# Kernel optimization log

Measured on AMD Instinct MI355X. Metric: run time of the kernel, lower is better.

## Reference

```python
import jax, jax.numpy as jnp
import numpy as np

P = 7            # cfg.POOLING_SIZE (= group_size)
N_CLASSES = 21   # PASCAL VOC incl. background
SPATIAL_SCALE = 1.0 / 16.0


def _round_half_up(x):
    # matches C round() for non-negative roi coords (jnp.round is banker's)
    return jnp.floor(x + 0.5)


def psroi_pool(feat, rois, out_dim):
    """Position-sensitive RoI average pooling via integral images.
    feat: [B, out_dim*P*P, H, W]; rois: [N, 5] (batch_idx, x1, y1, x2, y2).
    Returns [N, out_dim, P, P]."""
    B, C, H, W = feat.shape
    # summed-area table, zero-padded: S[b,c,h,w] = sum feat[b,c,:h,:w]
    S = jnp.cumsum(jnp.cumsum(feat, axis=2), axis=3)
    S = jnp.pad(S, ((0, 0), (0, 0), (1, 0), (1, 0)))

    b = rois[:, 0].astype(jnp.int32)
    x1 = _round_half_up(rois[:, 1]) * SPATIAL_SCALE
    y1 = _round_half_up(rois[:, 2]) * SPATIAL_SCALE
    x2 = _round_half_up(rois[:, 3] + 1.0) * SPATIAL_SCALE
    y2 = _round_half_up(rois[:, 4] + 1.0) * SPATIAL_SCALE
    roi_w = jnp.maximum(x2 - x1, 0.1)
    roi_h = jnp.maximum(y2 - y1, 0.1)
    bin_w = roi_w / P
    bin_h = roi_h / P

    g = jnp.arange(P, dtype=feat.dtype)
    hs = jnp.clip(jnp.floor(g[None] * bin_h[:, None] + y1[:, None]), 0, H).astype(jnp.int32)        # [N,P]
    he = jnp.clip(jnp.ceil((g[None] + 1.0) * bin_h[:, None] + y1[:, None]), 0, H).astype(jnp.int32)
    ws = jnp.clip(jnp.floor(g[None] * bin_w[:, None] + x1[:, None]), 0, W).astype(jnp.int32)
    we = jnp.clip(jnp.ceil((g[None] + 1.0) * bin_w[:, None] + x1[:, None]), 0, W).astype(jnp.int32)

    # channel for (ctop, gh, gw) is (ctop*P + gh)*P + gw == arange(C) reshaped
    c = jnp.arange(C, dtype=jnp.int32).reshape(1, out_dim, P, P)
    bi = b[:, None, None, None]
    h0 = hs[:, None, :, None]; h1 = he[:, None, :, None]
    w0 = ws[:, None, None, :]; w1 = we[:, None, None, :]
    # box-sum from integral image -> [N, out_dim, P, P]
    ssum = S[bi, c, h1, w1] - S[bi, c, h0, w1] - S[bi, c, h1, w0] + S[bi, c, h0, w0]

    dh = jnp.maximum(he - hs, 0)[:, None, :, None]
    dw = jnp.maximum(we - ws, 0)[:, None, None, :]
    area = (dh * dw).astype(feat.dtype)
    return jnp.where(area > 0, ssum / jnp.maximum(area, 1.0), 0.0)


def setup_inputs() -> dict:
    key = jax.random.key(0)
    k1, k2, k3, k4, k5 = jax.random.split(key, 5)
    B, Cin, H, W = 4, 2048, 64, 64
    base_feat = jax.random.normal(k1, (B, Cin, H, W), jnp.float32)
    w_conv1 = 0.01 * jax.random.normal(k2, (1024, Cin), jnp.float32)
    w_cls = 0.01 * jax.random.normal(k3, (N_CLASSES * P * P, 1024), jnp.float32)
    w_bbox = 0.001 * jax.random.normal(k4, (4 * N_CLASSES * P * P, 1024), jnp.float32)
    # 300 ROIs per image in image coords (image size = 16*H = 1024)
    n_per = 300
    ka, kb = jax.random.split(k5)
    xy1 = jax.random.uniform(ka, (B * n_per, 2), jnp.float32, 0.0, 900.0)
    wh = jax.random.uniform(kb, (B * n_per, 2), jnp.float32, 16.0, 160.0)
    xy2 = jnp.minimum(xy1 + wh, 1023.0)
    bidx = jnp.repeat(jnp.arange(B, dtype=jnp.float32), n_per)[:, None]
    rois = jnp.concatenate([bidx, xy1[:, 0:1], xy1[:, 1:2], xy2[:, 0:1], xy2[:, 1:2]], axis=1)
    return {"base_feat": base_feat, "rois": rois, "w_conv1": w_conv1, "w_cls": w_cls, "w_bbox": w_bbox}


def reference(base_feat, rois, w_conv1, w_cls, w_bbox):
    B = base_feat.shape[0]
    n_per = rois.shape[0] // B
    # 1x1 conv (no bias) + relu
    x = jax.nn.relu(jnp.einsum('oi,bihw->bohw', w_conv1, base_feat))
    # cls branch: 1x1 conv -> PSRoIPool -> PxP avgpool -> softmax
    cls_feat = jnp.einsum('oi,bihw->bohw', w_cls, x)
    pooled_cls = psroi_pool(cls_feat, rois, N_CLASSES)        # [N, 21, P, P]
    cls_score = pooled_cls.mean(axis=(2, 3))                   # [N, 21]
    cls_prob = jax.nn.softmax(cls_score, axis=1)
    # bbox branch: 1x1 conv -> PSRoIPool -> PxP avgpool
    bbox_feat = jnp.einsum('oi,bihw->bohw', w_bbox, x)
    pooled_loc = psroi_pool(bbox_feat, rois, 4 * N_CLASSES)    # [N, 84, P, P]
    bbox_pred = pooled_loc.mean(axis=(2, 3))                    # [N, 84]
    return cls_prob.reshape(B, n_per, -1), bbox_pred.reshape(B, n_per, -1)
```

## Files before the change

kernel.cpp:

```cpp
#include <hip/hip_runtime.h>
#include <cstdint>


typedef __attribute__((ext_vector_type(8))) short short8;
typedef __attribute__((ext_vector_type(4))) short short4v;
typedef __attribute__((ext_vector_type(4))) float f32x4;

#define OFF_FEATT 0ull
#define OFF_W1    67108864ull
#define OFF_X     71303168ull
#define OFF_WC    104857600ull
#define OFF_DESC  117702656ull
#define OFF_P     0ull

__device__ __forceinline__ unsigned short f2bf(float f) {
  unsigned u = __float_as_uint(f);
  u += 0x7fffu + ((u >> 16) & 1u);
  return (unsigned short)(u >> 16);
}
__device__ __forceinline__ float bf2f(unsigned short h) {
  return __uint_as_float(((unsigned)h) << 16);
}

__device__ __forceinline__ int swz6(int k6, int key) {
  return ((((k6 >> 3) & 7) ^ key) << 3) | (k6 & 7);
}

__device__ __forceinline__ void gload16(const void* g, void* l) {
  __builtin_amdgcn_global_load_lds((const __attribute__((address_space(1))) void*)g,
                                   (__attribute__((address_space(3))) void*)l, 16, 0, 0);
}

__global__ __launch_bounds__(256) void k_prep(const float* __restrict__ w_conv1,
                                              const float* __restrict__ wcls,
                                              const float* __restrict__ wbbox,
                                              const float* __restrict__ rois,
                                              const float* __restrict__ base_feat,
                                              unsigned short* __restrict__ w1b,
                                              unsigned short* __restrict__ Wc,
                                              int* __restrict__ desc,
                                              unsigned short* __restrict__ featT) {
  __shared__ float tile2[2][64][65];
  int bid = blockIdx.x;
  if (bid < 2048) {
    int t = bid * 256 + threadIdx.x;
    long e = (long)t * 4;
    int o = (int)(e >> 11), k = (int)(e & 2047);
    float4 q = *(const float4*)(w_conv1 + e);
    short4v s = {(short)f2bf(q.x), (short)f2bf(q.y), (short)f2bf(q.z), (short)f2bf(q.w)};
    int kp = (k & ~63) | swz6(k & 63, o & 7);
    *(short4v*)(w1b + (size_t)o * 2048 + kp) = s;
  } else if (bid < 8320) {
    int t = (bid - 2048) * 256 + threadIdx.x;
    size_t e = (size_t)t * 4;
    int c = (int)(e / 50176);
    int rem = (int)(e - (size_t)c * 50176);
    int ij = rem >> 10, k = rem & 1023;
    float4 q = make_float4(0.f, 0.f, 0.f, 0.f);
    if (c < 21)       q = *(const float4*)(wcls + (size_t)(c * 49 + ij) * 1024 + k);
    else if (c < 105) q = *(const float4*)(wbbox + (size_t)((c - 21) * 49 + ij) * 1024 + k);
    short4v s = {(short)f2bf(q.x), (short)f2bf(q.y), (short)f2bf(q.z), (short)f2bf(q.w)};
    int kp = (k & ~63) | swz6(k & 63, c & 7);
    *(short4v*)(Wc + ((size_t)(c * 49 + ij) * 1024 + kp)) = s;
  } else if (bid < 8565) {
    int t = (bid - 8320) * 256 + threadIdx.x;
    if (t >= 1280 * 49) return;
    int roi = t / 49, ij = t - roi * 49;
    int* d = desc + (size_t)t * 8;
    if (roi >= 1200) { d[0] = 0; d[1] = 0; d[2] = 0; d[3] = 0; d[4] = 0; ((float*)d)[5] = 0.f; return; }
    const float* r = rois + (size_t)roi * 5;
    int b = (int)r[0];
    float x1 = __fmul_rn(floorf(__fadd_rn(r[1], 0.5f)), 0.0625f);
    float y1 = __fmul_rn(floorf(__fadd_rn(r[2], 0.5f)), 0.0625f);
    float x2 = __fmul_rn(floorf(__fadd_rn(__fadd_rn(r[3], 1.0f), 0.5f)), 0.0625f);
    float y2 = __fmul_rn(floorf(__fadd_rn(__fadd_rn(r[4], 1.0f), 0.5f)), 0.0625f);
    float bw = __fdiv_rn(fmaxf(__fsub_rn(x2, x1), 0.1f), 7.0f);
    float bh = __fdiv_rn(fmaxf(__fsub_rn(y2, y1), 0.1f), 7.0f);
    int i = ij / 7, j = ij - (ij / 7) * 7;
    float fi = (float)i, fj = (float)j;
    int hs = (int)fminf(fmaxf(floorf(__fadd_rn(__fmul_rn(fi, bh), y1)), 0.f), 64.f);
    int he = (int)fminf(fmaxf(ceilf(__fadd_rn(__fmul_rn(__fadd_rn(fi, 1.f), bh), y1)), 0.f), 64.f);
    int wsx = (int)fminf(fmaxf(floorf(__fadd_rn(__fmul_rn(fj, bw), x1)), 0.f), 64.f);
    int we = (int)fminf(fmaxf(ceilf(__fadd_rn(__fmul_rn(__fadd_rn(fj, 1.f), bw), x1)), 0.f), 64.f);
    int dh = max(he - hs, 0), dw = max(we - wsx, 0);
    float inv = (dh * dw > 0) ? 1.0f / (float)(dh * dw) : 0.f;
    d[0] = b; d[1] = hs; d[2] = he; d[3] = wsx; d[4] = we;
    ((float*)d)[5] = inv;
  } else {
    int t = bid - 8565;
    int s0 = (t & 31) * 128;
    int c0 = ((t >> 5) & 31) * 64;
    int b = t >> 10;
    int tx4 = (threadIdx.x & 15) * 4;
    int cl0 = threadIdx.x >> 4;
    const float* sp = base_feat + ((size_t)b * 2048 + c0) * 4096 + s0;
    float4 q[8];
#pragma unroll
    for (int tt = 0; tt < 2; tt++)
#pragma unroll
      for (int i = 0; i < 4; i++) {
        int cl = i * 16 + cl0;
        q[tt * 4 + i] = *(const float4*)(sp + (size_t)cl * 4096 + tt * 64 + tx4);
      }
#pragma unroll
    for (int tt = 0; tt < 2; tt++)
#pragma unroll
      for (int i = 0; i < 4; i++)
        *(float4*)&tile2[tt][i * 16 + cl0][tx4] = q[tt * 4 + i];
    __syncthreads();
    int c8 = (threadIdx.x & 7) * 8;
    int sy = threadIdx.x >> 3;
#pragma unroll
    for (int tt = 0; tt < 2; tt++) {
      unsigned short* dp = featT + ((size_t)b * 4096 + s0 + tt * 64) * 2048 + c0;
#pragma unroll
      for (int i = 0; i < 2; i++) {
        int sl = i * 32 + sy;
        int key = sl & 7;
        short8 v = {(short)f2bf(tile2[tt][c8 + 0][sl]), (short)f2bf(tile2[tt][c8 + 1][sl]),
                    (short)f2bf(tile2[tt][c8 + 2][sl]), (short)f2bf(tile2[tt][c8 + 3][sl]),
                    (short)f2bf(tile2[tt][c8 + 4][sl]), (short)f2bf(tile2[tt][c8 + 5][sl]),
                    (short)f2bf(tile2[tt][c8 + 6][sl]), (short)f2bf(tile2[tt][c8 + 7][sl])};
        *(short8*)(dp + (size_t)sl * 2048 + ((((c8 >> 3) ^ key) << 3))) = v;
      }
    }
  }
}

__global__ __launch_bounds__(512, 2) void k_gemm_conv1(const short* __restrict__ A,
                                                       const short* __restrict__ Bw,
                                                       unsigned short* __restrict__ X) {
  __shared__ short lds[9 * 8192];
  int mt = blockIdx.x, nt = blockIdx.y;
  int tid = threadIdx.x, lane = tid & 63, wave = tid >> 6;
  int wm = wave >> 2, wn = wave & 3;

  const short* Ab = A + (size_t)mt * 256 * 2048;
  const short* Bb = Bw + (size_t)nt * 256 * 2048;

  f32x4 acc[8][4];
#pragma unroll
  for (int i = 0; i < 8; i++)
#pragma unroll
    for (int j = 0; j < 4; j++) acc[i][j] = (f32x4){0.f, 0.f, 0.f, 0.f};

  int sr = tid >> 3;
  int sc = (tid & 7) * 8;
  auto stage_half = [&](int h) {
    if (h >= 128) return;
    int kind = h & 3, tl = h >> 2, slot = h % 9;
    const short* src = ((kind & 2) ? Bb : Ab)
                     + (size_t)((kind & 1) * 128 + sr) * 2048 + tl * 64 + sc;
    char* dst = (char*)lds + slot * 16384 + tid * 16;
    gload16(src, dst);
    gload16(src + (size_t)64 * 2048, dst + 8192);
  };

#pragma unroll
  for (int h = 0; h < 5; h++) stage_half(h);

  int la15 = lane & 15;
  int key = lane & 7;
  int ko0 = (((lane >> 4)) ^ key) << 3;
  int ko1 = ((4 | (lane >> 4)) ^ key) << 3;
  int bro = (wn & 1) * 64;

  for (int t = 0; t < 32; ++t) {
    if (t < 31) asm volatile("s_waitcnt vmcnt(2)" ::: "memory");
    else        asm volatile("s_waitcnt vmcnt(0)" ::: "memory");
    __builtin_amdgcn_s_barrier();
    __builtin_amdgcn_sched_barrier(0);
    const short* Asl = lds + (size_t)((4 * t + wm) % 9) * 8192;
    const short* Bsl = lds + (size_t)((4 * t + 2 + (wn >> 1)) % 9) * 8192;
    short8 af[4], bf[4];

    stage_half(4 * t + 5);
#pragma unroll
    for (int j = 0; j < 4; j++)
      bf[j] = *(const short8*)(Bsl + (bro + j * 16 + la15) * 64 + ko0);
#pragma unroll
    for (int i = 0; i < 4; i++)
      af[i] = *(const short8*)(Asl + (i * 16 + la15) * 64 + ko0);
    __builtin_amdgcn_s_setprio(1);
#pragma unroll
    for (int i = 0; i < 4; i++)
#pragma unroll
      for (int j = 0; j < 4; j++)
        acc[i][j] = __builtin_amdgcn_mfma_f32_16x16x32_bf16(af[i], bf[j], acc[i][j], 0, 0, 0);
    __builtin_amdgcn_s_setprio(0);

    stage_half(4 * t + 6);
#pragma unroll
    for (int i = 0; i < 4; i++)
      af[i] = *(const short8*)(Asl + (64 + i * 16 + la15) * 64 + ko0);
    __builtin_amdgcn_s_setprio(1);
#pragma unroll
    for (int i = 0; i < 4; i++)
#pragma unroll
      for (int j = 0; j < 4; j++)
        acc[4 + i][j] = __builtin_amdgcn_mfma_f32_16x16x32_bf16(af[i], bf[j], acc[4 + i][j], 0, 0, 0);
    __builtin_amdgcn_s_setprio(0);

    stage_half(4 * t + 7);
#pragma unroll
    for (int j = 0; j < 4; j++)
      bf[j] = *(const short8*)(Bsl + (bro + j * 16 + la15) * 64 + ko1);
#pragma unroll
    for (int i = 0; i < 4; i++)
      af[i] = *(const short8*)(Asl + (i * 16 + la15) * 64 + ko1);
    __builtin_amdgcn_s_setprio(1);
#pragma unroll
    for (int i = 0; i < 4; i++)
#pragma unroll
      for (int j = 0; j < 4; j++)
        acc[i][j] = __builtin_amdgcn_mfma_f32_16x16x32_bf16(af[i], bf[j], acc[i][j], 0, 0, 0);
    __builtin_amdgcn_s_setprio(0);

    stage_half(4 * t + 8);
#pragma unroll
    for (int i = 0; i < 4; i++)
      af[i] = *(const short8*)(Asl + (64 + i * 16 + la15) * 64 + ko1);
    __builtin_amdgcn_s_setprio(1);
#pragma unroll
    for (int i = 0; i < 4; i++)
#pragma unroll
      for (int j = 0; j < 4; j++)
        acc[4 + i][j] = __builtin_amdgcn_mfma_f32_16x16x32_bf16(af[i], bf[j], acc[4 + i][j], 0, 0, 0);
    __builtin_amdgcn_s_setprio(0);
  }

  unsigned short* Xo = X + ((size_t)(mt * 256 + wm * 128)) * 1024 + nt * 256 + wn * 64;
#pragma unroll
  for (int ii = 0; ii < 8; ii++)
#pragma unroll
    for (int j = 0; j < 4; j++) {
      int row = ii * 16 + (lane >> 4) * 4;
      int col = j * 16 + la15;
#pragma unroll
      for (int r = 0; r < 4; r++)
        Xo[(size_t)(row + r) * 1024 + col] = f2bf(fmaxf(acc[ii][j][r], 0.f));
    }
}

__global__ __launch_bounds__(512) void k_fusedpool(const unsigned short* __restrict__ Xb,
                                                   const int* __restrict__ desc,
                                                   const unsigned short* __restrict__ Wc,
                                                   unsigned short* __restrict__ P,
                                                   int nroi) {
  int mt = blockIdx.x;
  int ij = blockIdx.y;
  int kh = blockIdx.z;
  __shared__ short As[64 * 64];
  __shared__ short Bs[128 * 64];
  __shared__ int dsc[64][4];
  int tid = threadIdx.x, lane = tid & 63, wave = tid >> 6;

  if (tid < 64) {
    const int* d = desc + ((size_t)(mt * 64 + tid) * 49 + ij) * 8;
    int b = d[0], hs = d[1], he = d[2], wsx = d[3], we = d[4];
    dsc[tid][0] = (b * 64 + hs) * 64 + wsx;
    dsc[tid][1] = max(he - hs, 0);
    dsc[tid][2] = max(we - wsx, 0);
    dsc[tid][3] = d[5];
  }
  __syncthreads();

  f32x4 acc[4];
#pragma unroll
  for (int i = 0; i < 4; i++) acc[i] = (f32x4){0.f, 0.f, 0.f, 0.f};

  const unsigned short* Bb = Wc + (size_t)ij * 1024;
  int lr = lane >> 3, lc = (lane & 7) * 8;
  int key = lane & 7;
  int la15 = lane & 15;
  int r64 = tid >> 3;
  int k8 = tid & 7;
  int cs = dsc[r64][0], dh = dsc[r64][1], dw = dsc[r64][2];
  float inv = __int_as_float(dsc[r64][3]);
  int aswz = r64 * 64 + ((k8 ^ (r64 & 7)) << 3);

  int kbeg = kh * 512, kend = kbeg + 512;
  for (int k0 = kbeg; k0 < kend; k0 += 64) {
    const unsigned short* xp = Xb + (size_t)cs * 1024 + k0 + k8 * 8;
    short8 v[9];
#pragma unroll
    for (int hh = 0; hh < 3; hh++)
#pragma unroll
      for (int ww = 0; ww < 3; ww++) {
        int ho = (hh < dh) ? hh : 0;
        int wo = (ww < dw) ? ww : 0;
        v[hh * 3 + ww] = *(const short8*)(xp + (size_t)(ho * 64 + wo) * 1024);
      }
    {
      int row = wave * 8 + lr;
      gload16(Bb + (size_t)row * (49 * 1024) + k0 + lc, (char*)Bs + wave * 1024);
      gload16(Bb + (size_t)(row + 64) * (49 * 1024) + k0 + lc, (char*)Bs + 8192 + wave * 1024);
    }
    float a0 = 0.f, a1 = 0.f, a2 = 0.f, a3 = 0.f;
    float a4 = 0.f, a5 = 0.f, a6 = 0.f, a7 = 0.f;
#pragma unroll
    for (int hh = 0; hh < 3; hh++)
#pragma unroll
      for (int ww = 0; ww < 3; ww++) {
        float m = ((hh < dh) && (ww < dw)) ? inv : 0.f;
        short8 vv = v[hh * 3 + ww];
        a0 = fmaf(m, bf2f((unsigned short)vv[0]), a0);
        a1 = fmaf(m, bf2f((unsigned short)vv[1]), a1);
        a2 = fmaf(m, bf2f((unsigned short)vv[2]), a2);
        a3 = fmaf(m, bf2f((unsigned short)vv[3]), a3);
        a4 = fmaf(m, bf2f((unsigned short)vv[4]), a4);
        a5 = fmaf(m, bf2f((unsigned short)vv[5]), a5);
        a6 = fmaf(m, bf2f((unsigned short)vv[6]), a6);
        a7 = fmaf(m, bf2f((unsigned short)vv[7]), a7);
      }
    short8 o = {(short)f2bf(a0), (short)f2bf(a1), (short)f2bf(a2), (short)f2bf(a3),
                (short)f2bf(a4), (short)f2bf(a5), (short)f2bf(a6), (short)f2bf(a7)};
    *(short8*)(As + aswz) = o;
    __syncthreads();
#pragma unroll
    for (int kt = 0; kt < 2; kt++) {
      int ko = (((kt << 2) | (lane >> 4)) ^ key) << 3;
      short8 bfr = *(const short8*)(Bs + (wave * 16 + la15) * 64 + ko);
      short8 af[4];
#pragma unroll
      for (int i = 0; i < 4; i++)
        af[i] = *(const short8*)(As + (i * 16 + la15) * 64 + ko);
#pragma unroll
      for (int i = 0; i < 4; i++)
        acc[i] = __builtin_amdgcn_mfma_f32_16x16x32_bf16(af[i], bfr, acc[i], 0, 0, 0);
    }
    __syncthreads();
  }
  unsigned short* Pb = P + (size_t)(kh * 49 + ij) * nroi * 112;
  int cc = wave * 16 + la15;
  if (cc < 112) {
#pragma unroll
    for (int i = 0; i < 4; i++) {
      int rbase = mt * 64 + i * 16 + (lane >> 4) * 4;
#pragma unroll
      for (int r = 0; r < 4; r++)
        Pb[(size_t)(rbase + r) * 112 + cc] = f2bf(acc[i][r]);
    }
  }
}

__global__ __launch_bounds__(128) void k_redfinal(const unsigned short* __restrict__ P,
                                                  float* __restrict__ out, int nroi) {
  int roi = blockIdx.x;
  int c = threadIdx.x;
  __shared__ float sc[112];
  __shared__ float es[32];
  if (c < 112) {
    const unsigned short* p = P + (size_t)roi * 112 + c;
    float s = 0.f;
#pragma unroll 7
    for (int ij = 0; ij < 98; ij++) s += bf2f(p[(size_t)ij * nroi * 112]);
    sc[c] = s * (1.f / 49.f);
  }
  __syncthreads();
  if (c < 21) {
    float mx = -1e30f;
#pragma unroll
    for (int k = 0; k < 21; k++) mx = fmaxf(mx, sc[k]);
    es[c] = expf(sc[c] - mx);
  }
  __syncthreads();
  if (c < 21) {
    float sum = 0.f;
#pragma unroll
    for (int k = 0; k < 21; k++) sum += es[k];
    float rs = 1.f / sum;
    out[(size_t)roi * 21 + c] = es[c] * rs;
  }
  if (c >= 21 && c < 105) {
    out[25200 + (size_t)roi * 84 + (c - 21)] = sc[c];
  }
}

extern "C" void kernel_launch(void* const* d_in, const int* in_sizes, int n_in,
                              void* d_out, int out_size, void* d_ws, size_t ws_size,
                              hipStream_t stream) {
  const float* base_feat = (const float*)d_in[0];
  const float* rois      = (const float*)d_in[1];
  const float* w_conv1   = (const float*)d_in[2];
  const float* w_cls     = (const float*)d_in[3];
  const float* w_bbox    = (const float*)d_in[4];
  float* out = (float*)d_out;
  char* ws = (char*)d_ws;

  unsigned short* featT = (unsigned short*)(ws + OFF_FEATT);
  unsigned short* w1b   = (unsigned short*)(ws + OFF_W1);
  unsigned short* X     = (unsigned short*)(ws + OFF_X);
  unsigned short* Wc    = (unsigned short*)(ws + OFF_WC);
  int*            desc  = (int*)(ws + OFF_DESC);
  unsigned short* P     = (unsigned short*)(ws + OFF_P);

  k_prep<<<12661, 256, 0, stream>>>(w_conv1, w_cls, w_bbox, rois, base_feat,
                                    w1b, Wc, desc, featT);
  k_gemm_conv1<<<dim3(64, 4), 512, 0, stream>>>((const short*)featT, (const short*)w1b, X);
  k_fusedpool<<<dim3(20, 49, 2), 512, 0, stream>>>(X, desc, Wc, P, 1280);
  k_redfinal<<<1200, 128, 0, stream>>>(P, out, 1280);
}
```

Baseline: 356.1 us.

## Double-buffer fused pool-GEMM loads with register prefetch and LDS ping-pong

Restructures the k-loop of the fused PSRoI pooling + GEMM kernel into a software pipeline. The next k-step's nine X gathers are prefetched into registers and the next B tile is written into an alternate LDS buffer while the current step computes. Fixed per-thread masks and offsets are hoisted out of the loop, and s_setprio is raised around the MFMAs. The intent is to hide global load latency behind compute. It doubles LDS use and register pressure, and relies on hand-written vmcnt waits whose correctness depends on exact load counts.

```diff
diff --git a/kernel.cpp b/kernel.cpp
--- a/kernel.cpp
+++ b/kernel.cpp
@@ -250,8 +250,8 @@
   int mt = blockIdx.x;
   int ij = blockIdx.y;
   int kh = blockIdx.z;
-  __shared__ short As[64 * 64];
-  __shared__ short Bs[128 * 64];
+  __shared__ short As[2 * 4096];
+  __shared__ short Bs[2 * 8192];
   __shared__ int dsc[64][4];
   int tid = threadIdx.x, lane = tid & 63, wave = tid >> 6;
 
@@ -278,58 +278,87 @@
   int cs = dsc[r64][0], dh = dsc[r64][1], dw = dsc[r64][2];
   float inv = __int_as_float(dsc[r64][3]);
   int aswz = r64 * 64 + ((k8 ^ (r64 & 7)) << 3);
-
-  int kbeg = kh * 512, kend = kbeg + 512;
-  for (int k0 = kbeg; k0 < kend; k0 += 64) {
-    const unsigned short* xp = Xb + (size_t)cs * 1024 + k0 + k8 * 8;
-    short8 v[9];
-#pragma unroll
-    for (int hh = 0; hh < 3; hh++)
-#pragma unroll
-      for (int ww = 0; ww < 3; ww++) {
-        int ho = (hh < dh) ? hh : 0;
-        int wo = (ww < dw) ? ww : 0;
-        v[hh * 3 + ww] = *(const short8*)(xp + (size_t)(ho * 64 + wo) * 1024);
-      }
-    {
-      int row = wave * 8 + lr;
-      gload16(Bb + (size_t)row * (49 * 1024) + k0 + lc, (char*)Bs + wave * 1024);
-      gload16(Bb + (size_t)(row + 64) * (49 * 1024) + k0 + lc, (char*)Bs + 8192 + wave * 1024);
-    }
+  int kbeg = kh * 512;
+
+  float mm[9];
+  int off[9];
+#pragma unroll
+  for (int hh = 0; hh < 3; hh++)
+#pragma unroll
+    for (int ww = 0; ww < 3; ww++) {
+      mm[hh * 3 + ww] = ((hh < dh) && (ww < dw)) ? inv : 0.f;
+      off[hh * 3 + ww] = (((hh < dh) ? hh : 0) * 64 + ((ww < dw) ? ww : 0)) * 1024;
+    }
+  const unsigned short* xbase = Xb + (size_t)cs * 1024 + kbeg + k8 * 8;
+
+  auto load9 = [&](short8* v, int kstep) {
+    const unsigned short* p = xbase + kstep * 64;
+#pragma unroll
+    for (int c = 0; c < 9; c++) v[c] = *(const short8*)(p + off[c]);
+  };
+  auto issueB = [&](int slot, int kstep) {
+    int row = wave * 8 + lr;
+    const unsigned short* src = Bb + (size_t)row * (49 * 1024) + kbeg + kstep * 64 + lc;
+    char* dst = (char*)Bs + slot * 16384 + wave * 1024;
+    gload16(src, dst);
+    gload16(src + (size_t)64 * (49 * 1024), dst + 8192);
+  };
+  auto avg_store = [&](short8* v, int slot) {
     float a0 = 0.f, a1 = 0.f, a2 = 0.f, a3 = 0.f;
     float a4 = 0.f, a5 = 0.f, a6 = 0.f, a7 = 0.f;
 #pragma unroll
-    for (int hh = 0; hh < 3; hh++)
-#pragma unroll
-      for (int ww = 0; ww < 3; ww++) {
-        float m = ((hh < dh) && (ww < dw)) ? inv : 0.f;
-        short8 vv = v[hh * 3 + ww];
-        a0 = fmaf(m, bf2f((unsigned short)vv[0]), a0);
-        a1 = fmaf(m, bf2f((unsigned short)vv[1]), a1);
-        a2 = fmaf(m, bf2f((unsigned short)vv[2]), a2);
-        a3 = fmaf(m, bf2f((unsigned short)vv[3]), a3);
-        a4 = fmaf(m, bf2f((unsigned short)vv[4]), a4);
-        a5 = fmaf(m, bf2f((unsigned short)vv[5]), a5);
-        a6 = fmaf(m, bf2f((unsigned short)vv[6]), a6);
-        a7 = fmaf(m, bf2f((unsigned short)vv[7]), a7);
-      }
+    for (int c = 0; c < 9; c++) {
+      float m = mm[c];
+      short8 vv = v[c];
+      a0 = fmaf(m, bf2f((unsigned short)vv[0]), a0);
+      a1 = fmaf(m, bf2f((unsigned short)vv[1]), a1);
+      a2 = fmaf(m, bf2f((unsigned short)vv[2]), a2);
+      a3 = fmaf(m, bf2f((unsigned short)vv[3]), a3);
+      a4 = fmaf(m, bf2f((unsigned short)vv[4]), a4);
+      a5 = fmaf(m, bf2f((unsigned short)vv[5]), a5);
+      a6 = fmaf(m, bf2f((unsigned short)vv[6]), a6);
+      a7 = fmaf(m, bf2f((unsigned short)vv[7]), a7);
+    }
     short8 o = {(short)f2bf(a0), (short)f2bf(a1), (short)f2bf(a2), (short)f2bf(a3),
                 (short)f2bf(a4), (short)f2bf(a5), (short)f2bf(a6), (short)f2bf(a7)};
-    *(short8*)(As + aswz) = o;
-    __syncthreads();
+    *(short8*)(As + slot * 4096 + aswz) = o;
+  };
+
+  short8 vA[9], vB[9];
+  load9(vA, 0);
+  issueB(0, 0);
+
+#pragma unroll
+  for (int t = 0; t < 8; t++) {
+    short8* cur = (t & 1) ? vB : vA;
+    short8* nxt = (t & 1) ? vA : vB;
+    if (t < 7) {
+      load9(nxt, t + 1);
+      asm volatile("s_waitcnt vmcnt(9)" ::: "memory");
+    } else {
+      asm volatile("s_waitcnt vmcnt(0)" ::: "memory");
+    }
+    __builtin_amdgcn_s_barrier();
+    if (t < 7) issueB((t + 1) & 1, t + 1);
+    avg_store(cur, t & 1);
+    asm volatile("s_waitcnt lgkmcnt(0)" ::: "memory");
+    __builtin_amdgcn_s_barrier();
+    const short* Asl = As + (t & 1) * 4096;
+    const short* Bsl = Bs + (t & 1) * 8192;
 #pragma unroll
     for (int kt = 0; kt < 2; kt++) {
       int ko = (((kt << 2) | (lane >> 4)) ^ key) << 3;
-      short8 bfr = *(const short8*)(Bs + (wave * 16 + la15) * 64 + ko);
+      short8 bfr = *(const short8*)(Bsl + (wave * 16 + la15) * 64 + ko);
       short8 af[4];
 #pragma unroll
       for (int i = 0; i < 4; i++)
-        af[i] = *(const short8*)(As + (i * 16 + la15) * 64 + ko);
+        af[i] = *(const short8*)(Asl + (i * 16 + la15) * 64 + ko);
+      __builtin_amdgcn_s_setprio(1);
 #pragma unroll
       for (int i = 0; i < 4; i++)
         acc[i] = __builtin_amdgcn_mfma_f32_16x16x32_bf16(af[i], bfr, acc[i], 0, 0, 0);
-    }
-    __syncthreads();
+      __builtin_amdgcn_s_setprio(0);
+    }
   }
   unsigned short* Pb = P + (size_t)(kh * 49 + ij) * nroi * 112;
   int cc = wave * 16 + la15;
```

Result: slower. 382.9 us (+7.5%).
